# Performance work log

Measured on AMD Instinct MI355X. Metric: run time of the kernel, lower is better.

Reference implementation:

```python
import jax, jax.numpy as jnp
import numpy as np

IN_SIZE = 1024
HID = 2048
OUT = 1024
M_STEPS = 100   # max extra ponder steps -> up to M_STEPS+1 total steps
EPS = 0.01


def setup_inputs() -> dict:
    key = jax.random.key(0)
    ks = jax.random.split(key, 11)
    inv = 1.0 / np.sqrt(HID)

    def unif(k, shape, scale):
        return jax.random.uniform(k, shape, jnp.float32, -scale, scale)

    return {
        "x": jax.random.normal(ks[0], (IN_SIZE,), jnp.float32),
        "h0": jax.random.normal(ks[1], (HID,), jnp.float32) * 0.1,
        "c0": jax.random.normal(ks[2], (HID,), jnp.float32) * 0.1,
        "W_ih": unif(ks[3], (4 * HID, 1 + IN_SIZE), inv),
        "b_ih": unif(ks[4], (4 * HID,), inv),
        "W_hh": unif(ks[5], (4 * HID, HID), inv),
        "b_hh": unif(ks[6], (4 * HID,), inv),
        "w_halt": unif(ks[7], (HID,), inv),
        "b_halt": jnp.ones((1,), jnp.float32),  # fc_halt.bias = 1.0 per source
        "W_out": unif(ks[8], (OUT, HID), inv),
        "b_out": unif(ks[9], (OUT,), inv),
    }


def reference(x, h0, c0, W_ih, b_ih, W_hh, b_hh, w_halt, b_halt, W_out, b_out):
    # Input contribution is constant across steps except the prepended halt flag
    # (1 on first step, 0 after). Precompute it once.
    ih_x = W_ih[:, 1:] @ x + b_ih + b_hh      # (4H,)
    w_flag = W_ih[:, 0]                        # (4H,)

    def step(carry, flag):
        h, c = carry
        gates = ih_x + flag * w_flag + W_hh @ h  # (4H,)
        i, f, g, o = jnp.split(gates, 4)
        i = jax.nn.sigmoid(i)
        f = jax.nn.sigmoid(f)
        g = jnp.tanh(g)
        o = jax.nn.sigmoid(o)
        c = f * c + i * g
        h = o * jnp.tanh(c)
        return (h, c), (h, c)

    flags = jnp.concatenate(
        [jnp.ones((1,), x.dtype), jnp.zeros((M_STEPS,), x.dtype)])
    _, (H, C) = jax.lax.scan(step, (h0, c0), flags)  # (M+1, HID) each

    p = jax.nn.sigmoid(H @ w_halt + b_halt[0])       # (M+1,) halting probs
    csum = jnp.cumsum(p)
    halted = csum >= 1.0 - EPS
    # n = first step where cumulative halt prob crosses threshold, capped at M
    n = jnp.where(jnp.any(halted), jnp.argmax(halted), M_STEPS)
    # remainder r = 1 - sum(p[:n]); csum[n] - p[n] == sum(p[:n])
    r = 1.0 - jnp.where(n > 0, csum[n] - p[n], 0.0)

    idx = jnp.arange(M_STEPS + 1)
    w = jnp.where(idx < n, p, jnp.where(idx == n, r, 0.0))  # (M+1,)

    outputs = H @ W_out.T + b_out                    # (M+1, OUT)
    output = w @ outputs                             # (OUT,) weights sum to 1
    h_out = w @ H                                    # (HID,)
    c_out = w @ C                                    # (HID,)
    ponder = n.astype(x.dtype) + 1.0 + r
    return output, (h_out, c_out), ponder
```

## Files before the change

kernel.cpp:

```cpp
#include <hip/hip_runtime.h>


#define HID    2048
#define INS    1024
#define OUTS   1024
#define MSTEPS 100
#define NBLK   256
#define NTHR   512
#define NWAVE  8
#define JPB    8
#define RPB    32
#define SLOTF  16

typedef unsigned long long u64;
typedef unsigned int u32;

__device__ __forceinline__ float wave_allreduce(float v) {
    #pragma unroll
    for (int off = 32; off > 0; off >>= 1)
        v += __shfl_xor(v, off, 64);
    return v;
}

__device__ __forceinline__ u32 bf16_2(float a, float b) {
    u32 ua = __float_as_uint(a), ub = __float_as_uint(b);
    ua = (ua + 0x7fffu + ((ua >> 16) & 1u)) >> 16;
    ub = (ub + 0x7fffu + ((ub >> 16) & 1u)) >> 16;
    return ua | (ub << 16);
}
__device__ __forceinline__ float blo(u32 u) { return __uint_as_float(u << 16); }
__device__ __forceinline__ float bhi(u32 u) { return __uint_as_float(u & 0xffff0000u); }

__device__ __forceinline__ u64 pack_tag(unsigned tag, float v) {
    return ((u64)tag << 32) | (u64)__float_as_uint(v);
}
__device__ __forceinline__ u64 aload(const u64* p) {
    return __hip_atomic_load(p, __ATOMIC_RELAXED, __HIP_MEMORY_SCOPE_AGENT);
}
__device__ __forceinline__ void astore(u64* p, u64 v) {
    __hip_atomic_store(p, v, __ATOMIC_RELAXED, __HIP_MEMORY_SCOPE_AGENT);
}


__global__ __launch_bounds__(NTHR, 2) void alstm_kernel(
    const float* __restrict__ x,      const float* __restrict__ h0,
    const float* __restrict__ c0,     const float* __restrict__ W_ih,
    const float* __restrict__ b_ih,   const float* __restrict__ W_hh,
    const float* __restrict__ b_hh,   const float* __restrict__ w_halt,
    const float* __restrict__ b_halt, const float* __restrict__ W_out,
    const float* __restrict__ b_out,  float* __restrict__ out,
    float* __restrict__ ws)
{
    const int b    = blockIdx.x;
    const int tid  = threadIdx.x;
    const int wave = tid >> 6;
    const int lane = tid & 63;

    float* arrive = ws;
    float* mail   = ws + NBLK * SLOTF;
    float* hbuf0  = ws + 2 * NBLK * SLOTF;
    float* hbuf1  = hbuf0 + HID;

    __shared__ u32   whh_u[RPB * 1024];
    __shared__ u32   hpk[HID / 2];
    __shared__ float x_lds[INS];
    __shared__ float hjoint[HID];
    __shared__ float gate_lds[RPB];
    __shared__ float ihx_lds[RPB];
    __shared__ float red_lds[4];
    __shared__ float bcast_lds;
    __shared__ float psum[NWAVE];

    const int j_own = b * JPB + tid;
    const int lr0   = 4 * wave;
    const int rbase = (lr0 >> 3) * HID + b * JPB + (lr0 & 7);

    #define SYNC_ROUND(tag_, part_, dot_) do {                                 \
        if (tid == 0) {                                                        \
            __threadfence();           \
            astore((u64*)(arrive + SLOTF * b), pack_tag((tag_), (part_)));     \
        }                                                                      \
        if (b == 0) {                                                          \
            float pf = 0.f;                                                    \
            if (tid < NBLK) {                                                  \
                u64 v = aload((u64*)(arrive + SLOTF * tid));                   \
                while ((unsigned)(v >> 32) != (unsigned)(tag_)) {              \
                    __builtin_amdgcn_s_sleep(1);                               \
                    v = aload((u64*)(arrive + SLOTF * tid));                   \
                }                                                              \
                pf = __uint_as_float((unsigned)v);                             \
            }                                                                  \
            float s = wave_allreduce(pf);                                      \
            if (lane == 0 && wave < 4) red_lds[wave] = s;                      \
            __syncthreads();                                                   \
            if (tid == 0)                                                      \
                bcast_lds = red_lds[0] + red_lds[1] + red_lds[2] + red_lds[3]; \
            __syncthreads();                                                   \
            if (tid < NBLK)                                                    \
                astore((u64*)(mail + SLOTF * tid), pack_tag((tag_), bcast_lds)); \
        }                                                                      \
        if (tid == 0) {                                                        \
            u64 v = aload((u64*)(mail + SLOTF * b));                           \
            while ((unsigned)(v >> 32) != (unsigned)(tag_)) {                  \
                __builtin_amdgcn_s_sleep(1);                                   \
                v = aload((u64*)(mail + SLOTF * b));                           \
            }                                                                  \
            bcast_lds = __uint_as_float((unsigned)v);                          \
            __threadfence();        \
        }                                                                      \
        __syncthreads();                                                       \
        (dot_) = bcast_lds;                                                    \
    } while (0)

    #define ISSUE_ROW(BUF, RR) do {                                           \
        const float4* src_ = (const float4*)(W_hh + (size_t)(rbase + (RR)) * HID); \
        _Pragma("unroll")                                                      \
        for (int m = 0; m < 8; ++m) BUF[m] = src_[lane + 64 * m];              \
    } while (0)

    #define CONVROW(BUF, RR, GACC) do {                                       \
        u32* dst_ = whh_u + (lr0 + (RR)) * (HID / 2);                         \
        const float4* h4_ = (const float4*)hjoint;                            \
        _Pragma("unroll")                                                      \
        for (int m = 0; m < 8; ++m) {                                         \
            float4 w4 = BUF[m];                                               \
            dst_[2 * (lane + 64 * m)]     = bf16_2(w4.x, w4.y);               \
            dst_[2 * (lane + 64 * m) + 1] = bf16_2(w4.z, w4.w);               \
            float4 hv_ = h4_[lane + 64 * m];                                  \
            GACC += w4.x * hv_.x + w4.y * hv_.y + w4.z * hv_.z + w4.w * hv_.w;\
        }                                                                      \
    } while (0)

    const float bh = b_halt[0];
    float2 xv  = ((const float2*)x)[tid];
    float4 h0v = ((const float4*)h0)[tid];
    float c_reg = (tid < JPB) ? c0[j_own]     : 0.f;
    float whv   = (tid < JPB) ? w_halt[j_own] : 0.f;
    float bo    = (tid < 4)   ? b_out[b * 4 + tid] : 0.f;
    float bsum = 0.f, wflg = 0.f;
    if (lane < 4) {
        const int lr = lr0 + lane;
        const int r  = (lr >> 3) * HID + b * JPB + (lr & 7);
        bsum = b_ih[r] + b_hh[r];
        wflg = W_ih[(size_t)r * (INS + 1)];
    }
    __builtin_amdgcn_sched_barrier(0);

    const int orow = b * 4 + (wave & 3);
    const int ohalf = wave >> 2;
    const float4* wrow = (const float4*)(W_out + (size_t)orow * HID) + ohalf * 256;
    float4 wo0 = wrow[lane], wo1 = wrow[lane + 64],
           wo2 = wrow[lane + 128], wo3 = wrow[lane + 192];

    const float*  wr_[4];
    const float4* wv_[4];
    int p0_[4];
    #pragma unroll
    for (int rr = 0; rr < 4; ++rr) {
        const int lr = lr0 + rr;
        const int r  = (lr >> 3) * HID + b * JPB + (lr & 7);
        wr_[rr] = W_ih + (size_t)r * (INS + 1) + 1;
        p0_[rr] = (4 - ((r + 1) & 3)) & 3;
        wv_[rr] = (const float4*)(wr_[rr] + p0_[rr]);
    }
    float4 iw0[4], iw1[4], iw2[4], iw3[4];
    #pragma unroll
    for (int ii = 0; ii < 4; ++ii) {
        const int i  = lane + 64 * ii;
        const int ic = (i < 255) ? i : 0;
        iw0[ii] = wv_[0][ic];
        iw1[ii] = wv_[1][ic];
        iw2[ii] = wv_[2][ic];
        iw3[ii] = wv_[3][ic];
    }

    float4 wa[8], wb[8];
    ISSUE_ROW(wa, 0);
    ISSUE_ROW(wb, 1);
    __builtin_amdgcn_sched_barrier(0);

    ((float2*)x_lds)[tid]  = xv;
    ((float4*)hjoint)[tid] = h0v;
    __syncthreads();

    float a0 = 0.f, a1 = 0.f, a2 = 0.f, a3 = 0.f;
    #pragma unroll
    for (int ii = 0; ii < 4; ++ii) {
        const int   i   = lane + 64 * ii;
        const int   ic  = (i < 255) ? i : 0;
        const float msk = (i < 255) ? 1.f : 0.f;
        #pragma unroll
        for (int rr = 0; rr < 4; ++rr) {
            float4 w4 = (rr == 0) ? iw0[ii] : (rr == 1) ? iw1[ii]
                      : (rr == 2) ? iw2[ii] : iw3[ii];
            const int k = p0_[rr] + 4 * ic;
            float s = w4.x * x_lds[k]     + w4.y * x_lds[k + 1]
                    + w4.z * x_lds[k + 2] + w4.w * x_lds[k + 3];
            s *= msk;
            if      (rr == 0) a0 += s;
            else if (rr == 1) a1 += s;
            else if (rr == 2) a2 += s;
            else              a3 += s;
        }
    }
    if (lane < 4) {
        #pragma unroll
        for (int rr = 0; rr < 4; ++rr) {
            const int p0 = p0_[rr];
            const int e  = (lane < p0) ? lane : 1020 + lane;
            float s = wr_[rr][e] * x_lds[e];
            if      (rr == 0) a0 += s;
            else if (rr == 1) a1 += s;
            else if (rr == 2) a2 += s;
            else              a3 += s;
        }
    }

    float g0 = 0.f, g1 = 0.f, g2 = 0.f, g3 = 0.f;
    CONVROW(wa, 0, g0);  ISSUE_ROW(wa, 2);
    CONVROW(wb, 1, g1);  ISSUE_ROW(wb, 3);
    CONVROW(wa, 2, g2);
    CONVROW(wb, 3, g3);

    a0 = wave_allreduce(a0); a1 = wave_allreduce(a1);
    a2 = wave_allreduce(a2); a3 = wave_allreduce(a3);
    g0 = wave_allreduce(g0); g1 = wave_allreduce(g1);
    g2 = wave_allreduce(g2); g3 = wave_allreduce(g3);
    if (lane < 4) {
        float av = (lane == 0) ? a0 : (lane == 1) ? a1 : (lane == 2) ? a2 : a3;
        float gv = (lane == 0) ? g0 : (lane == 1) ? g1 : (lane == 2) ? g2 : g3;
        ihx_lds[lr0 + lane]  = av + bsum;
        gate_lds[lr0 + lane] = av + bsum + wflg + gv;
    }
    __syncthreads();
    ((float4*)hjoint)[tid] = make_float4(0.f, 0.f, 0.f, 0.f);

    float h_reg = 0.f, cbar = 0.f;
    float csum = 0.f, r_halt = 0.f;
    int   n_halt = 0;
    for (int t = 0; t <= MSTEPS; ++t) {
        float part = 0.f;
        float* hdst = (t & 1) ? hbuf1 : hbuf0;
        if (tid < JPB) {
            float iv = gate_lds[0 * JPB + tid];
            float fv = gate_lds[1 * JPB + tid];
            float gv = gate_lds[2 * JPB + tid];
            float ov = gate_lds[3 * JPB + tid];
            iv = 1.f / (1.f + expf(-iv));
            fv = 1.f / (1.f + expf(-fv));
            gv = tanhf(gv);
            ov = 1.f / (1.f + expf(-ov));
            c_reg = fv * c_reg + iv * gv;
            h_reg = ov * tanhf(c_reg);
            hdst[j_own] = h_reg;
            part = h_reg * whv;
        }
        part += __shfl_down(part, 4, 64);
        part += __shfl_down(part, 2, 64);
        part += __shfl_down(part, 1, 64);

        float dotv;
        SYNC_ROUND(t + 1, part, dotv);

        float p = 1.f / (1.f + expf(-(dotv + bh)));
        float prev = csum;
        csum += p;
        bool  halt_now = (csum >= 1.f - 0.01f) || (t == MSTEPS);
        float wt = halt_now ? (1.f - prev) : p;

        float4 hv = ((const float4*)hdst)[tid];
        float4 hb = ((float4*)hjoint)[tid];
        hb.x += wt * hv.x; hb.y += wt * hv.y;
        hb.z += wt * hv.z; hb.w += wt * hv.w;
        ((float4*)hjoint)[tid] = hb;
        if (tid < JPB) cbar += wt * c_reg;
        if (halt_now) { n_halt = t; r_halt = 1.f - prev; break; }

        hpk[2 * tid]     = bf16_2(hv.x, hv.y);
        hpk[2 * tid + 1] = bf16_2(hv.z, hv.w);
        __syncthreads();

        {
            const uint4* hp = (const uint4*)hpk;
            float m0 = 0.f, m1 = 0.f, m2 = 0.f, m3 = 0.f;
            #pragma unroll
            for (int m = 0; m < 4; ++m) {
                uint4 hu = hp[lane + 64 * m];
                float h0a = blo(hu.x), h1a = bhi(hu.x);
                float h2a = blo(hu.y), h3a = bhi(hu.y);
                float h4a = blo(hu.z), h5a = bhi(hu.z);
                float h6a = blo(hu.w), h7a = bhi(hu.w);
                #pragma unroll
                for (int rr = 0; rr < 4; ++rr) {
                    const uint4* wp = (const uint4*)(whh_u + (lr0 + rr) * (HID / 2));
                    uint4 wu = wp[lane + 64 * m];
                    float s = blo(wu.x) * h0a + bhi(wu.x) * h1a
                            + blo(wu.y) * h2a + bhi(wu.y) * h3a
                            + blo(wu.z) * h4a + bhi(wu.z) * h5a
                            + blo(wu.w) * h6a + bhi(wu.w) * h7a;
                    if      (rr == 0) m0 += s;
                    else if (rr == 1) m1 += s;
                    else if (rr == 2) m2 += s;
                    else              m3 += s;
                }
            }
            m0 = wave_allreduce(m0); m1 = wave_allreduce(m1);
            m2 = wave_allreduce(m2); m3 = wave_allreduce(m3);
            if (lane < 4) {
                float mv = (lane == 0) ? m0 : (lane == 1) ? m1
                         : (lane == 2) ? m2 : m3;
                gate_lds[lr0 + lane] = ihx_lds[lr0 + lane] + mv;
            }
        }
        __syncthreads();
    }

    __syncthreads();
    if (tid < JPB) {
        out[OUTS + j_own]       = hjoint[j_own];
        out[OUTS + HID + j_own] = cbar;
    }
    if (b == 0 && tid == 0) out[OUTS + 2 * HID] = (float)(n_halt + 1) + r_halt;

    {
        const float4* hb4 = (const float4*)hjoint + ohalf * 256;
        float acc = 0.f;
        { float4 h4 = hb4[lane];       acc += wo0.x*h4.x + wo0.y*h4.y + wo0.z*h4.z + wo0.w*h4.w; }
        { float4 h4 = hb4[lane + 64];  acc += wo1.x*h4.x + wo1.y*h4.y + wo1.z*h4.z + wo1.w*h4.w; }
        { float4 h4 = hb4[lane + 128]; acc += wo2.x*h4.x + wo2.y*h4.y + wo2.z*h4.z + wo2.w*h4.w; }
        { float4 h4 = hb4[lane + 192]; acc += wo3.x*h4.x + wo3.y*h4.y + wo3.z*h4.z + wo3.w*h4.w; }
        acc = wave_allreduce(acc);
        if (lane == 0) psum[wave] = acc;
    }
    __syncthreads();
    if (tid < 4) out[b * 4 + tid] = psum[tid] + psum[tid + 4] + bo;

    #undef SYNC_ROUND
    #undef ISSUE_ROW
    #undef CONVROW
}

extern "C" void kernel_launch(void* const* d_in, const int* in_sizes, int n_in,
                              void* d_out, int out_size, void* d_ws, size_t ws_size,
                              hipStream_t stream) {
    const float* x      = (const float*)d_in[0];
    const float* h0     = (const float*)d_in[1];
    const float* c0     = (const float*)d_in[2];
    const float* W_ih   = (const float*)d_in[3];
    const float* b_ih   = (const float*)d_in[4];
    const float* W_hh   = (const float*)d_in[5];
    const float* b_hh   = (const float*)d_in[6];
    const float* w_halt = (const float*)d_in[7];
    const float* b_halt = (const float*)d_in[8];
    const float* W_out  = (const float*)d_in[9];
    const float* b_out  = (const float*)d_in[10];
    float* out = (float*)d_out;
    float* ws  = (float*)d_ws;

    hipMemsetAsync(d_ws, 0, 32768, stream);

    alstm_kernel<<<dim3(NBLK), dim3(NTHR), 0, stream>>>(
        x, h0, c0, W_ih, b_ih, W_hh, b_hh, w_halt, b_halt, W_out, b_out,
        out, ws);
}
```

Baseline: 168.7 us.

## Double block count and stream fp32 W_hh from cache instead of bf16 LDS copy

```diff
diff --git a/kernel.cpp b/kernel.cpp
--- a/kernel.cpp
+++ b/kernel.cpp
@@ -5,11 +5,11 @@
 #define INS    1024
 #define OUTS   1024
 #define MSTEPS 100
-#define NBLK   256
+#define NBLK   512
 #define NTHR   512
 #define NWAVE  8
-#define JPB    8
-#define RPB    32
+#define JPB    4
+#define RPB    16
 #define SLOTF  16
 
 typedef unsigned long long u64;
@@ -22,15 +22,6 @@
     return v;
 }
 
-__device__ __forceinline__ u32 bf16_2(float a, float b) {
-    u32 ua = __float_as_uint(a), ub = __float_as_uint(b);
-    ua = (ua + 0x7fffu + ((ua >> 16) & 1u)) >> 16;
-    ub = (ub + 0x7fffu + ((ub >> 16) & 1u)) >> 16;
-    return ua | (ub << 16);
-}
-__device__ __forceinline__ float blo(u32 u) { return __uint_as_float(u << 16); }
-__device__ __forceinline__ float bhi(u32 u) { return __uint_as_float(u & 0xffff0000u); }
-
 __device__ __forceinline__ u64 pack_tag(unsigned tag, float v) {
     return ((u64)tag << 32) | (u64)__float_as_uint(v);
 }
@@ -42,7 +33,7 @@
 }
 
 
-__global__ __launch_bounds__(NTHR, 2) void alstm_kernel(
+__global__ __launch_bounds__(NTHR, 4) void alstm_kernel(
     const float* __restrict__ x,      const float* __restrict__ h0,
     const float* __restrict__ c0,     const float* __restrict__ W_ih,
     const float* __restrict__ b_ih,   const float* __restrict__ W_hh,
@@ -61,19 +52,19 @@
     float* hbuf0  = ws + 2 * NBLK * SLOTF;
     float* hbuf1  = hbuf0 + HID;
 
-    __shared__ u32   whh_u[RPB * 1024];
-    __shared__ u32   hpk[HID / 2];
+    __shared__ float hcur[HID];
     __shared__ float x_lds[INS];
     __shared__ float hjoint[HID];
     __shared__ float gate_lds[RPB];
     __shared__ float ihx_lds[RPB];
-    __shared__ float red_lds[4];
+    __shared__ float red_lds[NWAVE];
     __shared__ float bcast_lds;
     __shared__ float psum[NWAVE];
 
     const int j_own = b * JPB + tid;
-    const int lr0   = 4 * wave;
-    const int rbase = (lr0 >> 3) * HID + b * JPB + (lr0 & 7);
+    const int lr0   = 2 * wave;
+    const int r0    = (lr0 >> 2) * HID + b * JPB + (lr0 & 3);
+    const int r1    = ((lr0 + 1) >> 2) * HID + b * JPB + ((lr0 + 1) & 3);
 
     #define SYNC_ROUND(tag_, part_, dot_) do {                                 \
         if (tid == 0) {                                                        \
@@ -82,7 +73,7 @@
         }                                                                      \
         if (b == 0) {                                                          \
             float pf = 0.f;                                                    \
-            if (tid < NBLK) {                                                  \
+            {                                                                  \
                 u64 v = aload((u64*)(arrive + SLOTF * tid));                   \
                 while ((unsigned)(v >> 32) != (unsigned)(tag_)) {              \
                     __builtin_amdgcn_s_sleep(1);                               \
@@ -91,13 +82,16 @@
                 pf = __uint_as_float((unsigned)v);                             \
             }                                                                  \
             float s = wave_allreduce(pf);                                      \
-            if (lane == 0 && wave < 4) red_lds[wave] = s;                      \
+            if (lane == 0) red_lds[wave] = s;                                  \
             __syncthreads();                                                   \
-            if (tid == 0)                                                      \
-                bcast_lds = red_lds[0] + red_lds[1] + red_lds[2] + red_lds[3]; \
+            if (tid == 0) {                                                    \
+                float tt = 0.f;                                                \
+                _Pragma("unroll")                                              \
+                for (int w_ = 0; w_ < NWAVE; ++w_) tt += red_lds[w_];          \
+                bcast_lds = tt;                                                \
+            }                                                                  \
             __syncthreads();                                                   \
-            if (tid < NBLK)                                                    \
-                astore((u64*)(mail + SLOTF * tid), pack_tag((tag_), bcast_lds)); \
+            astore((u64*)(mail + SLOTF * tid), pack_tag((tag_), bcast_lds));   \
         }                                                                      \
         if (tid == 0) {                                                        \
             u64 v = aload((u64*)(mail + SLOTF * b));                           \
@@ -112,123 +106,117 @@
         (dot_) = bcast_lds;                                                    \
     } while (0)
 
-    #define ISSUE_ROW(BUF, RR) do {                                           \
-        const float4* src_ = (const float4*)(W_hh + (size_t)(rbase + (RR)) * HID); \
-        _Pragma("unroll")                                                      \
-        for (int m = 0; m < 8; ++m) BUF[m] = src_[lane + 64 * m];              \
-    } while (0)
-
-    #define CONVROW(BUF, RR, GACC) do {                                       \
-        u32* dst_ = whh_u + (lr0 + (RR)) * (HID / 2);                         \
-        const float4* h4_ = (const float4*)hjoint;                            \
-        _Pragma("unroll")                                                      \
-        for (int m = 0; m < 8; ++m) {                                         \
-            float4 w4 = BUF[m];                                               \
-            dst_[2 * (lane + 64 * m)]     = bf16_2(w4.x, w4.y);               \
-            dst_[2 * (lane + 64 * m) + 1] = bf16_2(w4.z, w4.w);               \
-            float4 hv_ = h4_[lane + 64 * m];                                  \
-            GACC += w4.x * hv_.x + w4.y * hv_.y + w4.z * hv_.z + w4.w * hv_.w;\
-        }                                                                      \
-    } while (0)
-
     const float bh = b_halt[0];
     float2 xv  = ((const float2*)x)[tid];
     float4 h0v = ((const float4*)h0)[tid];
     float c_reg = (tid < JPB) ? c0[j_own]     : 0.f;
     float whv   = (tid < JPB) ? w_halt[j_own] : 0.f;
-    float bo    = (tid < 4)   ? b_out[b * 4 + tid] : 0.f;
+    float bo    = (tid < 2)   ? b_out[b * 2 + tid] : 0.f;
     float bsum = 0.f, wflg = 0.f;
-    if (lane < 4) {
+    if (lane < 2) {
         const int lr = lr0 + lane;
-        const int r  = (lr >> 3) * HID + b * JPB + (lr & 7);
+        const int r  = (lr >> 2) * HID + b * JPB + (lr & 3);
         bsum = b_ih[r] + b_hh[r];
         wflg = W_ih[(size_t)r * (INS + 1)];
     }
     __builtin_amdgcn_sched_barrier(0);
 
-    const int orow = b * 4 + (wave & 3);
-    const int ohalf = wave >> 2;
-    const float4* wrow = (const float4*)(W_out + (size_t)orow * HID) + ohalf * 256;
-    float4 wo0 = wrow[lane], wo1 = wrow[lane + 64],
-           wo2 = wrow[lane + 128], wo3 = wrow[lane + 192];
-
-    const float*  wr_[4];
-    const float4* wv_[4];
-    int p0_[4];
+    const float*  wr_[2];
+    const float4* wv_[2];
+    int p0_[2];
     #pragma unroll
-    for (int rr = 0; rr < 4; ++rr) {
+    for (int rr = 0; rr < 2; ++rr) {
         const int lr = lr0 + rr;
-        const int r  = (lr >> 3) * HID + b * JPB + (lr & 7);
+        const int r  = (lr >> 2) * HID + b * JPB + (lr & 3);
         wr_[rr] = W_ih + (size_t)r * (INS + 1) + 1;
         p0_[rr] = (4 - ((r + 1) & 3)) & 3;
         wv_[rr] = (const float4*)(wr_[rr] + p0_[rr]);
     }
-    float4 iw0[4], iw1[4], iw2[4], iw3[4];
+    float4 iw0[4], iw1[4];
     #pragma unroll
     for (int ii = 0; ii < 4; ++ii) {
         const int i  = lane + 64 * ii;
         const int ic = (i < 255) ? i : 0;
         iw0[ii] = wv_[0][ic];
         iw1[ii] = wv_[1][ic];
-        iw2[ii] = wv_[2][ic];
-        iw3[ii] = wv_[3][ic];
-    }
-
-    float4 wa[8], wb[8];
-    ISSUE_ROW(wa, 0);
-    ISSUE_ROW(wb, 1);
+    }
+
+    float4 wa[8];
+    {
+        const float4* src = (const float4*)(W_hh + (size_t)r0 * HID);
+        #pragma unroll
+        for (int m = 0; m < 8; ++m) wa[m] = src[lane + 64 * m];
+    }
+
+    const int orow = b * 2 + (wave & 1);
+    const int oq   = wave >> 1;
+    const float4* wrp = (const float4*)(W_out + (size_t)orow * HID) + oq * 128;
+    float4 wo0 = wrp[lane], wo1 = wrp[lane + 64];
+
     __builtin_amdgcn_sched_barrier(0);
 
     ((float2*)x_lds)[tid]  = xv;
     ((float4*)hjoint)[tid] = h0v;
     __syncthreads();
 
-    float a0 = 0.f, a1 = 0.f, a2 = 0.f, a3 = 0.f;
+    float a0 = 0.f, a1 = 0.f;
     #pragma unroll
     for (int ii = 0; ii < 4; ++ii) {
         const int   i   = lane + 64 * ii;
         const int   ic  = (i < 255) ? i : 0;
         const float msk = (i < 255) ? 1.f : 0.f;
-        #pragma unroll
-        for (int rr = 0; rr < 4; ++rr) {
-            float4 w4 = (rr == 0) ? iw0[ii] : (rr == 1) ? iw1[ii]
-                      : (rr == 2) ? iw2[ii] : iw3[ii];
-            const int k = p0_[rr] + 4 * ic;
-            float s = w4.x * x_lds[k]     + w4.y * x_lds[k + 1]
-                    + w4.z * x_lds[k + 2] + w4.w * x_lds[k + 3];
-            s *= msk;
-            if      (rr == 0) a0 += s;
-            else if (rr == 1) a1 += s;
-            else if (rr == 2) a2 += s;
-            else              a3 += s;
+        {
+            float4 w4 = iw0[ii];
+            const int k = p0_[0] + 4 * ic;
+            a0 += msk * (w4.x * x_lds[k]     + w4.y * x_lds[k + 1]
+                       + w4.z * x_lds[k + 2] + w4.w * x_lds[k + 3]);
+        }
+        {
+            float4 w4 = iw1[ii];
+            const int k = p0_[1] + 4 * ic;
+            a1 += msk * (w4.x * x_lds[k]     + w4.y * x_lds[k + 1]
+                       + w4.z * x_lds[k + 2] + w4.w * x_lds[k + 3]);
         }
     }
     if (lane < 4) {
         #pragma unroll
-        for (int rr = 0; rr < 4; ++rr) {
+        for (int rr = 0; rr < 2; ++rr) {
             const int p0 = p0_[rr];
             const int e  = (lane < p0) ? lane : 1020 + lane;
             float s = wr_[rr][e] * x_lds[e];
-            if      (rr == 0) a0 += s;
-            else if (rr == 1) a1 += s;
-            else if (rr == 2) a2 += s;
-            else              a3 += s;
-        }
-    }
-
-    float g0 = 0.f, g1 = 0.f, g2 = 0.f, g3 = 0.f;
-    CONVROW(wa, 0, g0);  ISSUE_ROW(wa, 2);
-    CONVROW(wb, 1, g1);  ISSUE_ROW(wb, 3);
-    CONVROW(wa, 2, g2);
-    CONVROW(wb, 3, g3);
+            if (rr == 0) a0 += s; else a1 += s;
+        }
+    }
+
+    float4 wb[8];
+    {
+        const float4* src = (const float4*)(W_hh + (size_t)r1 * HID);
+        #pragma unroll
+        for (int m = 0; m < 8; ++m) wb[m] = src[lane + 64 * m];
+    }
+
+    float g0 = 0.f, g1 = 0.f;
+    {
+        const float4* h4 = (const float4*)hjoint;
+        #pragma unroll
+        for (int m = 0; m < 8; ++m) {
+            float4 hh = h4[lane + 64 * m];
+            float4 w4 = wa[m];
+            g0 += w4.x * hh.x + w4.y * hh.y + w4.z * hh.z + w4.w * hh.w;
+        }
+        #pragma unroll
+        for (int m = 0; m < 8; ++m) {
+            float4 hh = h4[lane + 64 * m];
+            float4 w4 = wb[m];
+            g1 += w4.x * hh.x + w4.y * hh.y + w4.z * hh.z + w4.w * hh.w;
+        }
+    }
 
     a0 = wave_allreduce(a0); a1 = wave_allreduce(a1);
-    a2 = wave_allreduce(a2); a3 = wave_allreduce(a3);
     g0 = wave_allreduce(g0); g1 = wave_allreduce(g1);
-    g2 = wave_allreduce(g2); g3 = wave_allreduce(g3);
-    if (lane < 4) {
-        float av = (lane == 0) ? a0 : (lane == 1) ? a1 : (lane == 2) ? a2 : a3;
-        float gv = (lane == 0) ? g0 : (lane == 1) ? g1 : (lane == 2) ? g2 : g3;
+    if (lane < 2) {
+        float av = lane ? a1 : a0;
+        float gv = lane ? g1 : g0;
         ihx_lds[lr0 + lane]  = av + bsum;
         gate_lds[lr0 + lane] = av + bsum + wflg + gv;
     }
@@ -255,7 +243,6 @@
             hdst[j_own] = h_reg;
             part = h_reg * whv;
         }
-        part += __shfl_down(part, 4, 64);
         part += __shfl_down(part, 2, 64);
         part += __shfl_down(part, 1, 64);
 
@@ -276,39 +263,26 @@
         if (tid < JPB) cbar += wt * c_reg;
         if (halt_now) { n_halt = t; r_halt = 1.f - prev; break; }
 
-        hpk[2 * tid]     = bf16_2(hv.x, hv.y);
-        hpk[2 * tid + 1] = bf16_2(hv.z, hv.w);
+        ((float4*)hcur)[tid] = hv;
         __syncthreads();
 
         {
-            const uint4* hp = (const uint4*)hpk;
-            float m0 = 0.f, m1 = 0.f, m2 = 0.f, m3 = 0.f;
+            const float4* w0p = (const float4*)(W_hh + (size_t)r0 * HID);
+            const float4* w1p = (const float4*)(W_hh + (size_t)r1 * HID);
+            const float4* hc4 = (const float4*)hcur;
+            float m0 = 0.f, m1 = 0.f;
             #pragma unroll
-            for (int m = 0; m < 4; ++m) {
-                uint4 hu = hp[lane + 64 * m];
-                float h0a = blo(hu.x), h1a = bhi(hu.x);
-                float h2a = blo(hu.y), h3a = bhi(hu.y);
-                float h4a = blo(hu.z), h5a = bhi(hu.z);
-                float h6a = blo(hu.w), h7a = bhi(hu.w);
-                #pragma unroll
-                for (int rr = 0; rr < 4; ++rr) {
-                    const uint4* wp = (const uint4*)(whh_u + (lr0 + rr) * (HID / 2));
-                    uint4 wu = wp[lane + 64 * m];
-                    float s = blo(wu.x) * h0a + bhi(wu.x) * h1a
-                            + blo(wu.y) * h2a + bhi(wu.y) * h3a
-                            + blo(wu.z) * h4a + bhi(wu.z) * h5a
-                            + blo(wu.w) * h6a + bhi(wu.w) * h7a;
-                    if      (rr == 0) m0 += s;
-                    else if (rr == 1) m1 += s;
-                    else if (rr == 2) m2 += s;
-                    else              m3 += s;
-                }
+            for (int m = 0; m < 8; ++m) {
+                float4 wA = w0p[lane + 64 * m];
+                float4 wB = w1p[lane + 64 * m];
+                float4 hh = hc4[lane + 64 * m];
+                m0 += wA.x * hh.x + wA.y * hh.y + wA.z * hh.z + wA.w * hh.w;
+                m1 += wB.x * hh.x + wB.y * hh.y + wB.z * hh.z + wB.w * hh.w;
             }
-            m0 = wave_allreduce(m0); m1 = wave_allreduce(m1);
-            m2 = wave_allreduce(m2); m3 = wave_allreduce(m3);
-            if (lane < 4) {
-                float mv = (lane == 0) ? m0 : (lane == 1) ? m1
-                         : (lane == 2) ? m2 : m3;
+            m0 = wave_allreduce(m0);
+            m1 = wave_allreduce(m1);
+            if (lane < 2) {
+                float mv = lane ? m1 : m0;
                 gate_lds[lr0 + lane] = ihx_lds[lr0 + lane] + mv;
             }
         }
@@ -323,21 +297,19 @@
     if (b == 0 && tid == 0) out[OUTS + 2 * HID] = (float)(n_halt + 1) + r_halt;
 
     {
-        const float4* hb4 = (const float4*)hjoint + ohalf * 256;
+        const float4* hb4 = (const float4*)hjoint + oq * 128;
         float acc = 0.f;
-        { float4 h4 = hb4[lane];       acc += wo0.x*h4.x + wo0.y*h4.y + wo0.z*h4.z + wo0.w*h4.w; }
-        { float4 h4 = hb4[lane + 64];  acc += wo1.x*h4.x + wo1.y*h4.y + wo1.z*h4.z + wo1.w*h4.w; }
-        { float4 h4 = hb4[lane + 128]; acc += wo2.x*h4.x + wo2.y*h4.y + wo2.z*h4.z + wo2.w*h4.w; }
-        { float4 h4 = hb4[lane + 192]; acc += wo3.x*h4.x + wo3.y*h4.y + wo3.z*h4.z + wo3.w*h4.w; }
+        { float4 h4 = hb4[lane];      acc += wo0.x*h4.x + wo0.y*h4.y + wo0.z*h4.z + wo0.w*h4.w; }
+        { float4 h4 = hb4[lane + 64]; acc += wo1.x*h4.x + wo1.y*h4.y + wo1.z*h4.z + wo1.w*h4.w; }
         acc = wave_allreduce(acc);
         if (lane == 0) psum[wave] = acc;
     }
     __syncthreads();
-    if (tid < 4) out[b * 4 + tid] = psum[tid] + psum[tid + 4] + bo;
+    if (tid < 2)
+        out[b * 2 + tid] = psum[tid] + psum[tid + 2] + psum[tid + 4]
+                         + psum[tid + 6] + bo;
 
     #undef SYNC_ROUND
-    #undef ISSUE_ROW
-    #undef CONVROW
 }
 
 extern "C" void kernel_launch(void* const* d_in, const int* in_sizes, int n_in,
@@ -357,7 +329,7 @@
     float* out = (float*)d_out;
     float* ws  = (float*)d_ws;
 
-    hipMemsetAsync(d_ws, 0, 32768, stream);
+    hipMemsetAsync(d_ws, 0, 65536, stream);
 
     alstm_kernel<<<dim3(NBLK), dim3(NTHR), 0, stream>>>(
         x, h0, c0, W_ih, b_ih, W_hh, b_hh, w_halt, b_halt, W_out, b_out,
```

Result: slower. 208.3 us (+23.5%).

## Keep W_hh rows resident in fp32 registers instead of bf16 LDS copy

Applied to the files above, without the earlier changes.

```diff
diff --git a/kernel.cpp b/kernel.cpp
--- a/kernel.cpp
+++ b/kernel.cpp
@@ -22,15 +22,6 @@
     return v;
 }
 
-__device__ __forceinline__ u32 bf16_2(float a, float b) {
-    u32 ua = __float_as_uint(a), ub = __float_as_uint(b);
-    ua = (ua + 0x7fffu + ((ua >> 16) & 1u)) >> 16;
-    ub = (ub + 0x7fffu + ((ub >> 16) & 1u)) >> 16;
-    return ua | (ub << 16);
-}
-__device__ __forceinline__ float blo(u32 u) { return __uint_as_float(u << 16); }
-__device__ __forceinline__ float bhi(u32 u) { return __uint_as_float(u & 0xffff0000u); }
-
 __device__ __forceinline__ u64 pack_tag(unsigned tag, float v) {
     return ((u64)tag << 32) | (u64)__float_as_uint(v);
 }
@@ -42,7 +33,10 @@
 }
 
 
-__global__ __launch_bounds__(NTHR, 2) void alstm_kernel(
+__global__
+__attribute__((amdgpu_flat_work_group_size(NTHR, NTHR)))
+__attribute__((amdgpu_waves_per_eu(2, 2)))
+void alstm_kernel(
     const float* __restrict__ x,      const float* __restrict__ h0,
     const float* __restrict__ c0,     const float* __restrict__ W_ih,
     const float* __restrict__ b_ih,   const float* __restrict__ W_hh,
@@ -61,10 +55,9 @@
     float* hbuf0  = ws + 2 * NBLK * SLOTF;
     float* hbuf1  = hbuf0 + HID;
 
-    __shared__ u32   whh_u[RPB * 1024];
-    __shared__ u32   hpk[HID / 2];
     __shared__ float x_lds[INS];
     __shared__ float hjoint[HID];
+    __shared__ float hcur[HID];
     __shared__ float gate_lds[RPB];
     __shared__ float ihx_lds[RPB];
     __shared__ float red_lds[4];
@@ -112,22 +105,15 @@
         (dot_) = bcast_lds;                                                    \
     } while (0)
 
-    #define ISSUE_ROW(BUF, RR) do {                                           \
-        const float4* src_ = (const float4*)(W_hh + (size_t)(rbase + (RR)) * HID); \
+    #define DOT4(H4P, G0, G1, G2, G3) do {                                     \
+        const float4* h4__ = (H4P);                                            \
         _Pragma("unroll")                                                      \
-        for (int m = 0; m < 8; ++m) BUF[m] = src_[lane + 64 * m];              \
-    } while (0)
-
-    #define CONVROW(BUF, RR, GACC) do {                                       \
-        u32* dst_ = whh_u + (lr0 + (RR)) * (HID / 2);                         \
-        const float4* h4_ = (const float4*)hjoint;                            \
-        _Pragma("unroll")                                                      \
-        for (int m = 0; m < 8; ++m) {                                         \
-            float4 w4 = BUF[m];                                               \
-            dst_[2 * (lane + 64 * m)]     = bf16_2(w4.x, w4.y);               \
-            dst_[2 * (lane + 64 * m) + 1] = bf16_2(w4.z, w4.w);               \
-            float4 hv_ = h4_[lane + 64 * m];                                  \
-            GACC += w4.x * hv_.x + w4.y * hv_.y + w4.z * hv_.z + w4.w * hv_.w;\
+        for (int m = 0; m < 8; ++m) {                                          \
+            float4 hh = h4__[lane + 64 * m];                                   \
+            G0 += wa0[m].x*hh.x + wa0[m].y*hh.y + wa0[m].z*hh.z + wa0[m].w*hh.w; \
+            G1 += wa1[m].x*hh.x + wa1[m].y*hh.y + wa1[m].z*hh.z + wa1[m].w*hh.w; \
+            G2 += wa2[m].x*hh.x + wa2[m].y*hh.y + wa2[m].z*hh.z + wa2[m].w*hh.w; \
+            G3 += wa3[m].x*hh.x + wa3[m].y*hh.y + wa3[m].z*hh.z + wa3[m].w*hh.w; \
         }                                                                      \
     } while (0)
 
@@ -146,12 +132,6 @@
     }
     __builtin_amdgcn_sched_barrier(0);
 
-    const int orow = b * 4 + (wave & 3);
-    const int ohalf = wave >> 2;
-    const float4* wrow = (const float4*)(W_out + (size_t)orow * HID) + ohalf * 256;
-    float4 wo0 = wrow[lane], wo1 = wrow[lane + 64],
-           wo2 = wrow[lane + 128], wo3 = wrow[lane + 192];
-
     const float*  wr_[4];
     const float4* wv_[4];
     int p0_[4];
@@ -173,10 +153,29 @@
         iw2[ii] = wv_[2][ic];
         iw3[ii] = wv_[3][ic];
     }
-
-    float4 wa[8], wb[8];
-    ISSUE_ROW(wa, 0);
-    ISSUE_ROW(wb, 1);
+    __builtin_amdgcn_sched_barrier(0);
+
+    float4 wa0[8], wa1[8], wa2[8], wa3[8];
+    {
+        const float4* s0 = (const float4*)(W_hh + (size_t)(rbase + 0) * HID);
+        const float4* s1 = (const float4*)(W_hh + (size_t)(rbase + 1) * HID);
+        const float4* s2 = (const float4*)(W_hh + (size_t)(rbase + 2) * HID);
+        const float4* s3 = (const float4*)(W_hh + (size_t)(rbase + 3) * HID);
+        #pragma unroll
+        for (int m = 0; m < 8; ++m) {
+            wa0[m] = s0[lane + 64 * m];
+            wa1[m] = s1[lane + 64 * m];
+            wa2[m] = s2[lane + 64 * m];
+            wa3[m] = s3[lane + 64 * m];
+        }
+    }
+    __builtin_amdgcn_sched_barrier(0);
+
+    const int orow  = b * 4 + (wave & 3);
+    const int ohalf = wave >> 2;
+    const float4* wrow = (const float4*)(W_out + (size_t)orow * HID) + ohalf * 256;
+    float4 wo0 = wrow[lane], wo1 = wrow[lane + 64],
+           wo2 = wrow[lane + 128], wo3 = wrow[lane + 192];
     __builtin_amdgcn_sched_barrier(0);
 
     ((float2*)x_lds)[tid]  = xv;
@@ -217,10 +216,7 @@
     }
 
     float g0 = 0.f, g1 = 0.f, g2 = 0.f, g3 = 0.f;
-    CONVROW(wa, 0, g0);  ISSUE_ROW(wa, 2);
-    CONVROW(wb, 1, g1);  ISSUE_ROW(wb, 3);
-    CONVROW(wa, 2, g2);
-    CONVROW(wb, 3, g3);
+    DOT4((const float4*)hjoint, g0, g1, g2, g3);
 
     a0 = wave_allreduce(a0); a1 = wave_allreduce(a1);
     a2 = wave_allreduce(a2); a3 = wave_allreduce(a3);
@@ -276,34 +272,12 @@
         if (tid < JPB) cbar += wt * c_reg;
         if (halt_now) { n_halt = t; r_halt = 1.f - prev; break; }
 
-        hpk[2 * tid]     = bf16_2(hv.x, hv.y);
-        hpk[2 * tid + 1] = bf16_2(hv.z, hv.w);
+        ((float4*)hcur)[tid] = hv;
         __syncthreads();
 
         {
-            const uint4* hp = (const uint4*)hpk;
             float m0 = 0.f, m1 = 0.f, m2 = 0.f, m3 = 0.f;
-            #pragma unroll
-            for (int m = 0; m < 4; ++m) {
-                uint4 hu = hp[lane + 64 * m];
-                float h0a = blo(hu.x), h1a = bhi(hu.x);
-                float h2a = blo(hu.y), h3a = bhi(hu.y);
-                float h4a = blo(hu.z), h5a = bhi(hu.z);
-                float h6a = blo(hu.w), h7a = bhi(hu.w);
-                #pragma unroll
-                for (int rr = 0; rr < 4; ++rr) {
-                    const uint4* wp = (const uint4*)(whh_u + (lr0 + rr) * (HID / 2));
-                    uint4 wu = wp[lane + 64 * m];
-                    float s = blo(wu.x) * h0a + bhi(wu.x) * h1a
-                            + blo(wu.y) * h2a + bhi(wu.y) * h3a
-                            + blo(wu.z) * h4a + bhi(wu.z) * h5a
-                            + blo(wu.w) * h6a + bhi(wu.w) * h7a;
-                    if      (rr == 0) m0 += s;
-                    else if (rr == 1) m1 += s;
-                    else if (rr == 2) m2 += s;
-                    else              m3 += s;
-                }
-            }
+            DOT4((const float4*)hcur, m0, m1, m2, m3);
             m0 = wave_allreduce(m0); m1 = wave_allreduce(m1);
             m2 = wave_allreduce(m2); m3 = wave_allreduce(m3);
             if (lane < 4) {
@@ -336,8 +310,7 @@
     if (tid < 4) out[b * 4 + tid] = psum[tid] + psum[tid + 4] + bo;
 
     #undef SYNC_ROUND
-    #undef ISSUE_ROW
-    #undef CONVROW
+    #undef DOT4
 }
 
 extern "C" void kernel_launch(void* const* d_in, const int* in_sizes, int n_in,
```

Result: no change. 167.8 us (-0.5%).
